# Performance work log

Measured on AMD Instinct MI355X. Metric: run time of the kernel, lower is better.

## Reference

```python
import jax, jax.numpy as jnp
import numpy as np

B, V = 4, 10242
N = B * V            # 40968 packed vertices
E_PER = 30720        # edges per mesh
HID = 128


def _bilinear_sample(fm, grid):
    """pytorch3d vert_align core: grid_sample(align_corners=True, bilinear).
    fm: [B,C,H,W], grid: [B,V,2] xy in [-1,1] -> [B,V,C]."""
    b_, c_, h_, w_ = fm.shape
    x = (grid[..., 0] + 1.0) * 0.5 * (w_ - 1)
    y = (grid[..., 1] + 1.0) * 0.5 * (h_ - 1)
    x0f, y0f = jnp.floor(x), jnp.floor(y)
    wx1, wy1 = x - x0f, y - y0f
    wx0, wy0 = 1.0 - wx1, 1.0 - wy1
    x0 = jnp.clip(x0f, 0, w_ - 1).astype(jnp.int32)
    x1 = jnp.clip(x0f + 1, 0, w_ - 1).astype(jnp.int32)
    y0 = jnp.clip(y0f, 0, h_ - 1).astype(jnp.int32)
    y1 = jnp.clip(y0f + 1, 0, h_ - 1).astype(jnp.int32)
    fmt = jnp.transpose(fm, (0, 2, 3, 1))  # [B,H,W,C]
    bi = jnp.arange(b_)[:, None]
    g = lambda yy, xx: fmt[bi, yy, xx]     # [B,V,C]
    return ((wy0 * wx0)[..., None] * g(y0, x0)
            + (wy0 * wx1)[..., None] * g(y0, x1)
            + (wy1 * wx0)[..., None] * g(y1, x0)
            + (wy1 * wx1)[..., None] * g(y1, x1))


def _graph_conv(x, edges, w0, b0, w1, b1):
    """pytorch3d GraphConv (undirected): W0 x_i + sum over both edge dirs of W1 x_j."""
    h0 = x @ w0 + b0
    h1 = x @ w1 + b1
    e0, e1 = edges[:, 0], edges[:, 1]
    agg = jnp.zeros_like(h0).at[e0].add(h1[e1]).at[e1].add(h1[e0])
    return h0 + agg


def setup_inputs() -> dict:
    key = jax.random.key(0)
    ks = jax.random.split(key, 20)
    s = 0.05
    # per-mesh edges, offset into packed index space
    e = jax.random.randint(ks[0], (B, E_PER, 2), 0, V)
    e = e + (jnp.arange(B) * V)[:, None, None]
    return {
        "feat1": jax.random.normal(ks[1], (B, 256, 56, 56), jnp.float32),
        "feat2": jax.random.normal(ks[2], (B, 512, 28, 28), jnp.float32),
        "feat3": jax.random.normal(ks[3], (B, 1024, 14, 14), jnp.float32),
        "feat4": jax.random.normal(ks[4], (B, 2048, 7, 7), jnp.float32),
        "aligned_verts": jax.random.uniform(ks[5], (B, V, 3), jnp.float32, -1.0, 1.0),
        "verts_packed": jax.random.normal(ks[6], (N, 3), jnp.float32),
        "image_enc": jax.random.normal(ks[7], (B, 256), jnp.float32),
        "edges": e.reshape(B * E_PER, 2).astype(jnp.int64),
        "bottleneck_w": jax.random.normal(ks[8], (3840, HID), jnp.float32) * s,
        "bottleneck_b": jnp.zeros((HID,), jnp.float32),
        "g0_w0": jax.random.normal(ks[9], (387, HID), jnp.float32) * s,
        "g0_b0": jnp.zeros((HID,), jnp.float32),
        "g0_w1": jax.random.normal(ks[10], (387, HID), jnp.float32) * s,
        "g0_b1": jnp.zeros((HID,), jnp.float32),
        "gw0": jax.random.normal(ks[11], (7, HID, HID), jnp.float32) * s,
        "gb0": jnp.zeros((7, HID), jnp.float32),
        "gw1": jax.random.normal(ks[12], (7, HID, HID), jnp.float32) * s,
        "gb1": jnp.zeros((7, HID), jnp.float32),
        "off_w": jax.random.normal(ks[13], (HID, 3), jnp.float32) * s,
        "off_b": jnp.zeros((3,), jnp.float32),
    }


def reference(feat1, feat2, feat3, feat4, aligned_verts, verts_packed, image_enc,
              edges, bottleneck_w, bottleneck_b, g0_w0, g0_b0, g0_w1, g0_b1,
              gw0, gb0, gw1, gb1, off_w, off_b):
    grid = aligned_verts[..., :2]  # vert_align uses xy only
    samp = jnp.concatenate([_bilinear_sample(f, grid)
                            for f in (feat1, feat2, feat3, feat4)], axis=-1)
    samp = samp.reshape(N, 3840)  # return_packed=True
    vfeat = jax.nn.relu(samp @ bottleneck_w + bottleneck_b)
    enc = jnp.repeat(image_enc, V, axis=0)  # repeat_interleave
    x = jnp.concatenate([vfeat, verts_packed, enc], axis=1)  # [N,387]
    x = jax.nn.relu(_graph_conv(x, edges, g0_w0, g0_b0, g0_w1, g0_b1))
    for i in range(7):
        x = jax.nn.relu(_graph_conv(x, edges, gw0[i], gb0[i], gw1[i], gb1[i]))
    return x @ off_w + off_b  # delta_v [N,3]
```

## Files before the change

### kernel.cpp

```cpp
#include <hip/hip_runtime.h>

static inline int ceil_div(int a, int b) { return (a + b - 1) / b; }

typedef __attribute__((ext_vector_type(8))) short short8;
typedef __attribute__((ext_vector_type(4))) float floatx4;

__device__ __forceinline__ unsigned short f2bf(float f) {
    unsigned int u = __float_as_uint(f);
    unsigned int r = (u + 0x7fffu + ((u >> 16) & 1u)) >> 16;
    return (unsigned short)r;
}
__device__ __forceinline__ float bf2f(unsigned short h) {
    return __uint_as_float(((unsigned int)h) << 16);
}

__global__ __launch_bounds__(1024) void scan1_k(const int* __restrict__ deg,
                                                int* __restrict__ excl,
                                                int* __restrict__ bsum, int Nv) {
    __shared__ int s[1024];
    int tid = threadIdx.x;
    int i = blockIdx.x * 1024 + tid;
    int v = (i < Nv) ? deg[i] : 0;
    s[tid] = v;
    __syncthreads();
    for (int off = 1; off < 1024; off <<= 1) {
        int t = (tid >= off) ? s[tid - off] : 0;
        __syncthreads();
        if (tid >= off) s[tid] += t;
        __syncthreads();
    }
    if (i < Nv) excl[i] = s[tid] - v;
    if (tid == 1023) bsum[blockIdx.x] = s[1023];
}

__global__ __launch_bounds__(1024) void scan3_k(const int* __restrict__ excl,
                                                const int* __restrict__ bsum,
                                                const int* __restrict__ deg,
                                                int* __restrict__ rowptr,
                                                int* __restrict__ cursor, int Nv, int nb) {
    __shared__ int offS;
    if (threadIdx.x < 64) {
        int v = (threadIdx.x < min((int)blockIdx.x, nb)) ? bsum[threadIdx.x] : 0;
#pragma unroll
        for (int m = 1; m < 64; m <<= 1) v += __shfl_xor(v, m);
        if (threadIdx.x == 0) offS = v;
    }
    __syncthreads();
    int i = blockIdx.x * 1024 + threadIdx.x;
    if (i < Nv) {
        int val = excl[i] + offS;
        rowptr[i] = val;
        cursor[i] = val;
        if (i == Nv - 1) rowptr[Nv] = val + deg[i];
    }
}

__global__ __launch_bounds__(256) void fill_adj_k(const int* __restrict__ edges,
                                                  int* __restrict__ cursor,
                                                  int* __restrict__ adj, int E) {
    int e = blockIdx.x * blockDim.x + threadIdx.x;
    if (e < E) {
        int a = edges[2 * e], b = edges[2 * e + 1];
        adj[atomicAdd(&cursor[a], 1)] = b;
        adj[atomicAdd(&cursor[b], 1)] = a;
    }
}

__global__ __launch_bounds__(256) void fatpre_k(
    const int* __restrict__ edges, int* __restrict__ deg, int E, int nE,
    const float* __restrict__ g0w0, const float* __restrict__ g0w1,
    const float* __restrict__ gw0, const float* __restrict__ gw1,
    unsigned short* __restrict__ Wt, const float* __restrict__ bw,
    unsigned short* __restrict__ bwT, const float* __restrict__ enc,
    float* __restrict__ encp, const float* __restrict__ fm1, const float* __restrict__ fm2,
    const float* __restrict__ fm3, const float* __restrict__ fm4,
    unsigned short* __restrict__ ft1, unsigned short* __restrict__ ft2,
    unsigned short* __restrict__ ft3, unsigned short* __restrict__ ft4, int B_) {
    __shared__ float tl[64][65];
    int bid = blockIdx.x;
    int tid = threadIdx.x;
    if (bid < nE) {
        int e = bid * 256 + tid;
        if (e < E) {
            atomicAdd(&deg[edges[2 * e]], 1);
            atomicAdd(&deg[edges[2 * e + 1]], 1);
        }
    } else if (bid < nE + 16) {
        int lh = bid - nE;
        int l = lh >> 1, h = lh & 1;
        const float* src;
        if (l == 0) src = h ? g0w1 : g0w0;
        else src = (h ? gw1 : gw0) + (size_t)(l - 1) * 16384;
        unsigned short* dst = Wt + (size_t)lh * 16384;
        for (int idx = tid; idx < 16384; idx += 256) {
            int n = idx >> 7, k = idx & 127;
            dst[n * 128 + k] = f2bf(src[k * 128 + n]);
        }
    } else if (bid < nE + 46) {
        int blk = bid - nE - 16;
        for (int idx = tid; idx < 16384; idx += 256) {
            int n = idx >> 7, kk = idx & 127;
            bwT[(size_t)n * 3840 + blk * 128 + kk] =
                f2bf(bw[(size_t)(blk * 128 + kk) * 128 + n]);
        }
    } else if (bid < nE + 46 + B_) {
        int b = bid - nE - 46;
        int sH = tid >> 7;
        int j = tid & 127;
        const float* w = sH ? g0w1 : g0w0;
        const float* eb = enc + b * 256;
        float acc = 0.f;
        for (int c = 0; c < 256; ++c) acc = fmaf(eb[c], w[(131 + c) * 128 + j], acc);
        encp[(sH * B_ + b) * 128 + j] = acc;
    } else {
        int idx = bid - (nE + 46 + B_);
        const float* fm;
        unsigned short* ft;
        int C, HW, PT, CT;
        int q1 = 49 * 4 * B_, q2 = 13 * 8 * B_, q3 = 4 * 16 * B_;
        if (idx < q1) {
            fm = fm1; ft = ft1; C = 256; HW = 3136; PT = 49; CT = 4;
        } else if ((idx -= q1) < q2) {
            fm = fm2; ft = ft2; C = 512; HW = 784; PT = 13; CT = 8;
        } else if ((idx -= q2) < q3) {
            fm = fm3; ft = ft3; C = 1024; HW = 196; PT = 4; CT = 16;
        } else {
            idx -= q3;
            fm = fm4; ft = ft4; C = 2048; HW = 49; PT = 1; CT = 32;
        }
        int ct = idx % CT;
        int r2 = idx / CT;
        int pt = r2 % PT;
        int b = r2 / PT;
        int p0 = pt * 64, c0 = ct * 64;
        const float* fb = fm + (size_t)b * C * HW;
#pragma unroll
        for (int l = 0; l < 4; ++l) {
            int i = tid + l * 256;
            int ch = i >> 4;
            int pq = (i & 15) * 4;
            const float* src = fb + (size_t)(c0 + ch) * HW + p0 + pq;
            float4 v;
            if (p0 + pq + 3 < HW) {
                v = *(const float4*)src;
            } else {
                v.x = (p0 + pq + 0 < HW) ? src[0] : 0.f;
                v.y = (p0 + pq + 1 < HW) ? src[1] : 0.f;
                v.z = (p0 + pq + 2 < HW) ? src[2] : 0.f;
                v.w = (p0 + pq + 3 < HW) ? src[3] : 0.f;
            }
            tl[ch][pq + 0] = v.x;
            tl[ch][pq + 1] = v.y;
            tl[ch][pq + 2] = v.z;
            tl[ch][pq + 3] = v.w;
        }
        __syncthreads();
#pragma unroll
        for (int l = 0; l < 2; ++l) {
            int i = tid + l * 256;
            int p = i >> 3;
            int cc = (i & 7) * 8;
            if (p0 + p < HW) {
                short8 o;
#pragma unroll
                for (int j = 0; j < 8; ++j) o[j] = (short)f2bf(tl[cc + j][p]);
                *(short8*)(ft + ((size_t)b * HW + p0 + p) * C + c0 + cc) = o;
            }
        }
    }
}

__global__ __launch_bounds__(256) void proj_all_k(
    const unsigned short* __restrict__ ft1, const unsigned short* __restrict__ ft2,
    const unsigned short* __restrict__ ft3, const unsigned short* __restrict__ ft4,
    const unsigned short* __restrict__ bwT, float* __restrict__ o1, float* __restrict__ o2,
    float* __restrict__ o3, float* __restrict__ o4, int B_) {
    __shared__ unsigned short wlds[8192];

    int tid = threadIdx.x;
    int n1 = 49 * B_ * 2, n2 = 13 * B_ * 2, n3 = 4 * B_ * 4;
    int bid = blockIdx.x;
    const unsigned short* ft;
    float* op;
    int C, HW, PT, idx, koff, KB;
    if (bid < n1) {
        ft = ft1; op = o1; C = 256; HW = 3136; PT = 49; idx = bid; koff = 0; KB = 128;
    } else if (bid < n1 + n2) {
        ft = ft2; op = o2; C = 512; HW = 784; PT = 13; idx = bid - n1; koff = 256; KB = 256;
    } else if (bid < n1 + n2 + n3) {
        ft = ft3; op = o3; C = 1024; HW = 196; PT = 4; idx = bid - n1 - n2; koff = 768;
        KB = 256;
    } else {
        ft = ft4; op = o4; C = 2048; HW = 49; PT = 1; idx = bid - n1 - n2 - n3; koff = 1792;
        KB = 256;
    }
    int pt = idx % PT;
    int r2 = idx / PT;
    int b = r2 % B_;
    int zz = r2 / B_;
    int p0 = pt * 64;
    int kcf0 = zz * KB;

    int wave = tid >> 6, lane = tid & 63;
    int row16 = lane & 15, quad = lane >> 4;
    int p = p0 + wave * 16 + row16;
    bool pok = (p < HW);
    int pc = pok ? p : (HW - 1);
    const unsigned short* frow = ft + ((size_t)b * HW + pc) * C;

    floatx4 acc[8];
#pragma unroll
    for (int j = 0; j < 8; ++j) acc[j] = (floatx4){0.f, 0.f, 0.f, 0.f};

    int nzz = KB >> 6;
    for (int zz2 = 0; zz2 < nzz; ++zz2) {
        int kcf = kcf0 + zz2 * 64;
        int kcw = koff + kcf;
        if (zz2) __syncthreads();
#pragma unroll
        for (int l = 0; l < 4; ++l) {
            int i2 = tid + l * 256;
            int n = i2 >> 3, c16 = i2 & 7;
            *(short8*)&wlds[n * 64 + ((c16 ^ (n & 7)) * 8)] =
                *(const short8*)(bwT + (size_t)n * 3840 + kcw + c16 * 8);
        }
        short8 ax[2];
#pragma unroll
        for (int ks = 0; ks < 2; ++ks)
            ax[ks] = *(const short8*)(frow + kcf + ks * 32 + quad * 8);
        __syncthreads();
#pragma unroll
        for (int ks = 0; ks < 2; ++ks) {
            int c = ks * 4 + quad;
#pragma unroll
            for (int nt = 0; nt < 8; ++nt) {
                int wr = nt * 16 + row16;
                short8 bwf = *(short8*)&wlds[wr * 64 + ((c ^ (wr & 7)) * 8)];
                acc[nt] =
                    __builtin_amdgcn_mfma_f32_16x16x32_bf16(ax[ks], bwf, acc[nt], 0, 0, 0);
            }
        }
    }

    float* obase = op + (size_t)b * HW * 128;
#pragma unroll
    for (int nt = 0; nt < 8; ++nt) {
        int colg = nt * 16 + row16;
#pragma unroll
        for (int rr = 0; rr < 4; ++rr) {
            int pr = p0 + wave * 16 + quad * 4 + rr;
            if (pr < HW) atomicAdd(&obase[(size_t)pr * 128 + colg], acc[nt][rr]);
        }
    }
}

__device__ __forceinline__ void sample2(const float* __restrict__ pp, int Hh, int Ww,
                                        float gx, float gy, int c2, float& a0, float& a1) {
    float x = (gx + 1.f) * 0.5f * (float)(Ww - 1);
    float y = (gy + 1.f) * 0.5f * (float)(Hh - 1);
    float x0f = floorf(x), y0f = floorf(y);
    float wx1 = x - x0f, wy1 = y - y0f;
    float wx0 = 1.f - wx1, wy0 = 1.f - wy1;
    int x0 = (int)fminf(fmaxf(x0f, 0.f), (float)(Ww - 1));
    int x1 = (int)fminf(fmaxf(x0f + 1.f, 0.f), (float)(Ww - 1));
    int y0 = (int)fminf(fmaxf(y0f, 0.f), (float)(Hh - 1));
    int y1 = (int)fminf(fmaxf(y0f + 1.f, 0.f), (float)(Hh - 1));
    float2 r00 = *(const float2*)(pp + (size_t)(y0 * Ww + x0) * 128 + c2);
    float2 r01 = *(const float2*)(pp + (size_t)(y0 * Ww + x1) * 128 + c2);
    float2 r10 = *(const float2*)(pp + (size_t)(y1 * Ww + x0) * 128 + c2);
    float2 r11 = *(const float2*)(pp + (size_t)(y1 * Ww + x1) * 128 + c2);
    a0 += wy0 * (wx0 * r00.x + wx1 * r01.x) + wy1 * (wx0 * r10.x + wx1 * r11.x);
    a1 += wy0 * (wx0 * r00.y + wx1 * r01.y) + wy1 * (wx0 * r10.y + wx1 * r11.y);
}

__global__ __launch_bounds__(256) void sample_bottleneck_k(
    const float* __restrict__ av, const float* __restrict__ pp1, const float* __restrict__ pp2,
    const float* __restrict__ pp3, const float* __restrict__ pp4, const float* __restrict__ bb,
    const float* __restrict__ verts, const float* __restrict__ encp,
    const float* __restrict__ g0w0, const float* __restrict__ g0w1,
    const float* __restrict__ g0b0, const float* __restrict__ g0b1,
    unsigned short* __restrict__ X, unsigned short* __restrict__ H, int Nv, int V_, int B_) {
    int wave = threadIdx.x >> 6, lane = threadIdx.x & 63;
    int n = blockIdx.x * 4 + wave;
    if (n >= Nv) return;
    int b = n / V_;
    int c2 = 2 * lane;
    float gx = av[(size_t)n * 3 + 0];
    float gy = av[(size_t)n * 3 + 1];
    float2 bbv = *(const float2*)(bb + c2);
    float a0 = bbv.x, a1 = bbv.y;
    sample2(pp1 + (size_t)b * 3136 * 128, 56, 56, gx, gy, c2, a0, a1);
    sample2(pp2 + (size_t)b * 784 * 128, 28, 28, gx, gy, c2, a0, a1);
    sample2(pp3 + (size_t)b * 196 * 128, 14, 14, gx, gy, c2, a0, a1);
    sample2(pp4 + (size_t)b * 49 * 128, 7, 7, gx, gy, c2, a0, a1);
    *(unsigned int*)(X + (size_t)n * 128 + c2) =
        (unsigned int)f2bf(fmaxf(a0, 0.f)) | ((unsigned int)f2bf(fmaxf(a1, 0.f)) << 16);

    float v0 = verts[n * 3 + 0], v1 = verts[n * 3 + 1], v2 = verts[n * 3 + 2];
    float2 e0 = *(const float2*)(encp + ((size_t)(0 * B_ + b)) * 128 + c2);
    float2 e1 = *(const float2*)(encp + ((size_t)(1 * B_ + b)) * 128 + c2);
    float2 gb0v = *(const float2*)(g0b0 + c2);
    float2 gb1v = *(const float2*)(g0b1 + c2);
    float2 w0a = *(const float2*)(g0w0 + 128 * 128 + c2);
    float2 w0b = *(const float2*)(g0w0 + 129 * 128 + c2);
    float2 w0c = *(const float2*)(g0w0 + 130 * 128 + c2);
    float2 w1a = *(const float2*)(g0w1 + 128 * 128 + c2);
    float2 w1b = *(const float2*)(g0w1 + 129 * 128 + c2);
    float2 w1c = *(const float2*)(g0w1 + 130 * 128 + c2);
    float h0x = e0.x + gb0v.x + v0 * w0a.x + v1 * w0b.x + v2 * w0c.x;
    float h0y = e0.y + gb0v.y + v0 * w0a.y + v1 * w0b.y + v2 * w0c.y;
    float h1x = e1.x + gb1v.x + v0 * w1a.x + v1 * w1b.x + v2 * w1c.x;
    float h1y = e1.y + gb1v.y + v0 * w1a.y + v1 * w1b.y + v2 * w1c.y;
    *(unsigned int*)(H + (size_t)n * 256 + c2) =
        (unsigned int)f2bf(h0x) | ((unsigned int)f2bf(h0y) << 16);
    *(unsigned int*)(H + (size_t)n * 256 + 128 + c2) =
        (unsigned int)f2bf(h1x) | ((unsigned int)f2bf(h1y) << 16);
}

__global__ __launch_bounds__(256) void agg0_k(const unsigned short* __restrict__ X,
                                              const unsigned short* __restrict__ H,
                                              const int* __restrict__ rowptr,
                                              const int* __restrict__ adj,
                                              unsigned short* __restrict__ AggX,
                                              unsigned short* __restrict__ AggH, int Nv,
                                              int Etot) {
    int wave = threadIdx.x >> 6, lane = threadIdx.x & 63;
    int n0 = (blockIdx.x * 4 + wave) * 4;
    if (n0 >= Nv) return;
    int g = lane >> 4, c = lane & 15;
    int rp = rowptr[min(n0 + (lane & 7), Nv)];
    int sg = __shfl(rp, g);
    int eg = __shfl(rp, g + 1);
    int m = eg - sg;
    m = max(m, __shfl_xor(m, 16));
    m = max(m, __shfl_xor(m, 32));

    int n = n0 + g;
    bool nok = (n < Nv);
    int nc = nok ? n : (Nv - 1);
    float accx[8], acch[8];
    short8 h0v = *(const short8*)(H + (size_t)nc * 256 + c * 8);
#pragma unroll
    for (int j = 0; j < 8; ++j) {
        accx[j] = 0.f;
        acch[j] = bf2f((unsigned short)h0v[j]);
    }

    for (int it = 0; it < m; it += 8) {
        int t = sg + it + (lane & 7);
        int adjv = adj[min(t, Etot - 1)];
        short8 bx[8], bh[8];
#pragma unroll
        for (int q = 0; q < 8; ++q) {
            int nbq = __shfl(adjv, (lane & 48) + q);
            bx[q] = *(const short8*)(X + (size_t)nbq * 128 + c * 8);
            bh[q] = *(const short8*)(H + (size_t)nbq * 256 + 128 + c * 8);
        }
#pragma unroll
        for (int q = 0; q < 8; ++q) {
            bool ok = (sg + it + q < eg);
#pragma unroll
            for (int j = 0; j < 8; ++j) {
                accx[j] += ok ? bf2f((unsigned short)bx[q][j]) : 0.f;
                acch[j] += ok ? bf2f((unsigned short)bh[q][j]) : 0.f;
            }
        }
    }
    if (nok) {
        short8 ox, oh;
#pragma unroll
        for (int j = 0; j < 8; ++j) {
            ox[j] = (short)f2bf(accx[j]);
            oh[j] = (short)f2bf(acch[j]);
        }
        *(short8*)(AggX + (size_t)n * 128 + c * 8) = ox;
        *(short8*)(AggH + (size_t)n * 128 + c * 8) = oh;
    }
}

__global__ __launch_bounds__(256) void agg_x_k(const unsigned short* __restrict__ X,
                                               const int* __restrict__ rowptr,
                                               const int* __restrict__ adj,
                                               unsigned short* __restrict__ Agg, int Nv,
                                               int Etot) {
    int wave = threadIdx.x >> 6, lane = threadIdx.x & 63;
    int n0 = (blockIdx.x * 4 + wave) * 4;
    if (n0 >= Nv) return;
    int g = lane >> 4, c = lane & 15;
    int rp = rowptr[min(n0 + (lane & 7), Nv)];
    int sg = __shfl(rp, g);
    int eg = __shfl(rp, g + 1);
    int m = eg - sg;
    m = max(m, __shfl_xor(m, 16));
    m = max(m, __shfl_xor(m, 32));

    float acc[8];
#pragma unroll
    for (int j = 0; j < 8; ++j) acc[j] = 0.f;

    for (int it = 0; it < m; it += 8) {
        int t = sg + it + (lane & 7);
        int adjv = adj[min(t, Etot - 1)];
        short8 buf[8];
#pragma unroll
        for (int q = 0; q < 8; ++q) {
            int nbq = __shfl(adjv, (lane & 48) + q);
            buf[q] = *(const short8*)(X + (size_t)nbq * 128 + c * 8);
        }
#pragma unroll
        for (int q = 0; q < 8; ++q) {
            bool ok = (sg + it + q < eg);
#pragma unroll
            for (int j = 0; j < 8; ++j) {
                float v = bf2f((unsigned short)buf[q][j]);
                acc[j] += ok ? v : 0.f;
            }
        }
    }

    if (n0 + g < Nv) {
        short8 o;
#pragma unroll
        for (int j = 0; j < 8; ++j) o[j] = (short)f2bf(acc[j]);
        *(short8*)(Agg + (size_t)(n0 + g) * 128 + c * 8) = o;
    }
}

__global__ __launch_bounds__(256, 3) void gemm_dual_k(
    const unsigned short* __restrict__ Xin, const unsigned short* __restrict__ Agg,
    const unsigned short* __restrict__ Wt,
    const float* __restrict__ b0, const float* __restrict__ b1,
    const unsigned short* __restrict__ aggh, const int* __restrict__ degv,
    unsigned short* __restrict__ Xout, int M, const float* __restrict__ ow,
    const float* __restrict__ ob, float* __restrict__ outp) {
    __shared__ unsigned short wlds[16384];
    __shared__ unsigned short cs[64 * 72];
    __shared__ float bS[128];
    __shared__ float owS[192];

    int tid = threadIdx.x;
    int m0 = blockIdx.x * 128;
    int yb = blockIdx.y;

    int wave = tid >> 6, lane = tid & 63;
    int row16 = lane & 15;
    int quad = lane >> 4;
    int wrow = wave * 16;

    short8 axT[2][4], agT[2][4];
    int dgT[2][4];
    {
        int g = min(m0 + wrow + row16, M - 1);
#pragma unroll
        for (int ks = 0; ks < 4; ++ks) {
            int koff = ks * 32 + quad * 8;
            axT[0][ks] = *(const short8*)(Xin + (size_t)g * 128 + koff);
            agT[0][ks] = *(const short8*)(Agg + (size_t)g * 128 + koff);
        }
#pragma unroll
        for (int rr = 0; rr < 4; ++rr)
            dgT[0][rr] = degv[min(m0 + wrow + quad * 4 + rr, M - 1)];
    }

    if (tid < 64) {
        bS[tid] = b0 ? b0[yb * 64 + tid] : 0.f;
        bS[64 + tid] = b1 ? b1[yb * 64 + tid] : 0.f;
    }
    if (outp && tid < 192) owS[tid] = ow[yb * 192 + tid];

    const unsigned short* W0h = Wt + (size_t)yb * 64 * 128;
    const unsigned short* W1h = Wt + 16384 + (size_t)yb * 64 * 128;
#pragma unroll
    for (int l = 0; l < 8; ++l) {
        int idx = tid + l * 256;
        int half = idx >> 10;
        int r = (idx >> 4) & 63;
        int c16 = idx & 15;
        int sw = (c16 ^ (r & 15)) * 8;
        const unsigned short* src = (half ? W1h : W0h) + r * 128 + c16 * 8;
        *(short8*)&wlds[half * 8192 + r * 128 + sw] = *(const short8*)src;
    }
    __syncthreads();

    {
        int g = min(m0 + 64 + wrow + row16, M - 1);
#pragma unroll
        for (int ks = 0; ks < 4; ++ks) {
            int koff = ks * 32 + quad * 8;
            axT[1][ks] = *(const short8*)(Xin + (size_t)g * 128 + koff);
            agT[1][ks] = *(const short8*)(Agg + (size_t)g * 128 + koff);
        }
#pragma unroll
        for (int rr = 0; rr < 4; ++rr)
            dgT[1][rr] = degv[min(m0 + 64 + wrow + quad * 4 + rr, M - 1)];
    }

#pragma unroll
    for (int t = 0; t < 2; ++t) {
        int mT = m0 + t * 64;
        floatx4 acc[4];
#pragma unroll
        for (int j = 0; j < 4; j++) acc[j] = (floatx4){0.f, 0.f, 0.f, 0.f};

#pragma unroll
        for (int ks = 0; ks < 4; ++ks) {
            int c = ks * 4 + quad;
#pragma unroll
            for (int nt = 0; nt < 4; ++nt) {
                int wr = nt * 16 + row16;
                short8 bw0 = *(short8*)&wlds[wr * 128 + ((c ^ row16) * 8)];
                short8 bw1 = *(short8*)&wlds[8192 + wr * 128 + ((c ^ row16) * 8)];
                acc[nt] = __builtin_amdgcn_mfma_f32_16x16x32_bf16(axT[t][ks], bw0, acc[nt], 0, 0, 0);
                acc[nt] = __builtin_amdgcn_mfma_f32_16x16x32_bf16(agT[t][ks], bw1, acc[nt], 0, 0, 0);
            }
        }

        unsigned short cvs[4][4];
#pragma unroll
        for (int nt = 0; nt < 4; ++nt) {
            int colh = nt * 16 + row16;
            int colg = yb * 64 + colh;
            float bc0 = bS[colh];
            float bc1 = bS[64 + colh];
#pragma unroll
            for (int rr = 0; rr < 4; ++rr) {
                int row = wrow + quad * 4 + rr;
                int gm = mT + row;
                float v = acc[nt][rr] + bc0 + (float)dgT[t][rr] * bc1;
                if (aggh && gm < M) v += bf2f(aggh[(size_t)gm * 128 + colg]);
                unsigned short cv = f2bf(fmaxf(v, 0.f));
                cvs[nt][rr] = cv;
                cs[row * 72 + colh] = cv;
            }
        }

        if (outp) {
#pragma unroll
            for (int rr = 0; rr < 4; ++rr) {
                float h0 = 0.f, h1 = 0.f, h2 = 0.f;
#pragma unroll
                for (int nt = 0; nt < 4; ++nt) {
                    int colh = nt * 16 + row16;
                    float xv = bf2f(cvs[nt][rr]);
                    h0 += xv * owS[colh * 3 + 0];
                    h1 += xv * owS[colh * 3 + 1];
                    h2 += xv * owS[colh * 3 + 2];
                }
#pragma unroll
                for (int mm = 1; mm < 16; mm <<= 1) {
                    h0 += __shfl_xor(h0, mm);
                    h1 += __shfl_xor(h1, mm);
                    h2 += __shfl_xor(h2, mm);
                }
                if (row16 == 0) {
                    int gm = mT + wrow + quad * 4 + rr;
                    if (gm < M) {
                        float e0 = (yb == 0) ? ob[0] : 0.f;
                        float e1 = (yb == 0) ? ob[1] : 0.f;
                        float e2 = (yb == 0) ? ob[2] : 0.f;
                        atomicAdd(&outp[gm * 3 + 0], h0 + e0);
                        atomicAdd(&outp[gm * 3 + 1], h1 + e1);
                        atomicAdd(&outp[gm * 3 + 2], h2 + e2);
                    }
                }
            }
        }
        __syncthreads();

        {
            int r = tid >> 2;
            int cq = (tid & 3) * 16;
            int gm = mT + r;
            if (gm < M) {
                unsigned short* dst = Xout + (size_t)gm * 128 + yb * 64 + cq;
                *(short8*)dst = *(short8*)&cs[r * 72 + cq];
                *(short8*)(dst + 8) = *(short8*)&cs[r * 72 + cq + 8];
            }
        }
        __syncthreads();
    }
}

extern "C" void kernel_launch(void* const* d_in, const int* in_sizes, int n_in, void* d_out,
                              int out_size, void* d_ws, size_t ws_size, hipStream_t stream) {
    const float* feat1 = (const float*)d_in[0];
    const float* feat2 = (const float*)d_in[1];
    const float* feat3 = (const float*)d_in[2];
    const float* feat4 = (const float*)d_in[3];
    const float* av = (const float*)d_in[4];
    const float* verts = (const float*)d_in[5];
    const float* image_enc = (const float*)d_in[6];
    const int* edges = (const int*)d_in[7];
    const float* bw = (const float*)d_in[8];
    const float* bb = (const float*)d_in[9];
    const float* g0w0 = (const float*)d_in[10];
    const float* g0b0 = (const float*)d_in[11];
    const float* g0w1 = (const float*)d_in[12];
    const float* g0b1 = (const float*)d_in[13];
    const float* gw0 = (const float*)d_in[14];
    const float* gb0 = (const float*)d_in[15];
    const float* gw1 = (const float*)d_in[16];
    const float* gb1 = (const float*)d_in[17];
    const float* off_w = (const float*)d_in[18];
    const float* off_b = (const float*)d_in[19];

    int B_ = in_sizes[6] / 256;
    int N_ = in_sizes[5] / 3;
    int V_ = N_ / B_;
    int E_ = in_sizes[7] / 2;

    char* wsb = (char*)d_ws;
    size_t off = 0;
    auto alloc = [&](size_t bytes) -> void* {
        void* p = (void*)(wsb + off);
        off += (bytes + 255) & ~(size_t)255;
        return p;
    };
    int S1 = B_ * 3136 * 128;
    int S2 = B_ * 784 * 128;
    int S3 = B_ * 196 * 128;
    int S4 = B_ * 49 * 128;
    float* pp1 = (float*)alloc((size_t)S1 * 4);
    float* pp2 = (float*)alloc((size_t)S2 * 4);
    float* pp3 = (float*)alloc((size_t)S3 * 4);
    float* pp4 = (float*)alloc((size_t)S4 * 4);
    size_t pp_bytes = off;
    unsigned short* fmT1 = (unsigned short*)alloc((size_t)B_ * 3136 * 256 * 2);
    unsigned short* fmT2 = (unsigned short*)alloc((size_t)B_ * 784 * 512 * 2);
    unsigned short* fmT3 = (unsigned short*)alloc((size_t)B_ * 196 * 1024 * 2);
    unsigned short* fmT4 = (unsigned short*)alloc((size_t)B_ * 49 * 2048 * 2);
    unsigned short* XA = (unsigned short*)alloc((size_t)N_ * 128 * 2);
    unsigned short* XB = (unsigned short*)alloc((size_t)N_ * 128 * 2);
    unsigned short* AggB = (unsigned short*)alloc((size_t)N_ * 128 * 2);
    unsigned short* AggH = (unsigned short*)alloc((size_t)N_ * 128 * 2);
    unsigned short* Hb = (unsigned short*)alloc((size_t)N_ * 256 * 2);
    unsigned short* Wt = (unsigned short*)alloc((size_t)8 * 2 * 128 * 128 * 2);
    unsigned short* bwT = (unsigned short*)alloc((size_t)128 * 3840 * 2);
    float* encp = (float*)alloc((size_t)2 * B_ * 128 * 4);
    int* deg = (int*)alloc((size_t)(N_ + 1) * 4);
    int* rowptr = (int*)alloc((size_t)(N_ + 1) * 4);
    int* cursor = (int*)alloc((size_t)N_ * 4);
    int* excl = (int*)alloc((size_t)N_ * 4);
    int* bsum = (int*)alloc((size_t)64 * 4);
    int* adj = (int*)alloc((size_t)2 * E_ * 4);

    hipMemsetAsync(deg, 0, (N_ + 1) * sizeof(int), stream);
    hipMemsetAsync(wsb, 0, pp_bytes, stream);
    hipMemsetAsync(d_out, 0, out_size, stream);

    int nE = ceil_div(E_, 256);
    int NT = (49 * 4 + 13 * 8 + 4 * 16 + 1 * 32) * B_;
    fatpre_k<<<nE + 46 + B_ + NT, 256, 0, stream>>>(
        edges, deg, E_, nE, g0w0, g0w1, gw0, gw1, Wt, bw, bwT, image_enc, encp, feat1, feat2,
        feat3, feat4, fmT1, fmT2, fmT3, fmT4, B_);

    int nb = ceil_div(N_, 1024);
    scan1_k<<<nb, 1024, 0, stream>>>(deg, excl, bsum, N_);
    scan3_k<<<nb, 1024, 0, stream>>>(excl, bsum, deg, rowptr, cursor, N_, nb);
    fill_adj_k<<<ceil_div(E_, 256), 256, 0, stream>>>(edges, cursor, adj, E_);

    int nproj = 49 * B_ * 2 + 13 * B_ * 2 + 4 * B_ * 4 + 1 * B_ * 8;
    proj_all_k<<<nproj, 256, 0, stream>>>(fmT1, fmT2, fmT3, fmT4, bwT, pp1, pp2, pp3, pp4,
                                          B_);

    sample_bottleneck_k<<<ceil_div(N_, 4), 256, 0, stream>>>(
        av, pp1, pp2, pp3, pp4, bb, verts, encp, g0w0, g0w1, g0b0, g0b1, XA, Hb, N_, V_, B_);

    dim3 ggrid(ceil_div(N_, 128), 2);
    int agrid4 = ceil_div(N_, 16);
    agg0_k<<<agrid4, 256, 0, stream>>>(XA, Hb, rowptr, adj, AggB, AggH, N_, 2 * E_);
    gemm_dual_k<<<ggrid, 256, 0, stream>>>(XA, AggB, Wt, nullptr, nullptr, AggH, deg, XB, N_,
                                           nullptr, nullptr, nullptr);
    unsigned short* Xc = XB;
    unsigned short* Xn = XA;
    for (int i = 0; i < 7; ++i) {
        bool last = (i == 6);
        agg_x_k<<<agrid4, 256, 0, stream>>>(Xc, rowptr, adj, AggB, N_, 2 * E_);
        gemm_dual_k<<<ggrid, 256, 0, stream>>>(Xc, AggB, Wt + (size_t)(i + 1) * 32768,
                                               gb0 + i * 128, gb1 + i * 128, nullptr, deg, Xn,
                                               N_, last ? off_w : nullptr,
                                               last ? off_b : nullptr,
                                               last ? (float*)d_out : nullptr);
        unsigned short* t = Xc;
        Xc = Xn;
        Xn = t;
    }
}
```

Measured before the change: 436.1 us.

## Fuse seven graph-conv layers into one cooperative persistent kernel with grid syncs

Replaces the 14 separate aggregation and GEMM launches for layers 1-7 with a single cooperative kernel. It loops over the layers and separates the aggregation and GEMM phases with grid-wide syncs, using grid-stride loops over chunks and tiles. This removes per-launch overhead and the inter-kernel gaps. The trade-off is a grid limited by occupancy, grid-sync cost, and weights reloaded into LDS for every tile a block handles.

Measured after the change: 990.9 us. 127% more time.

```diff
diff --git a/kernel.cpp b/kernel.cpp
--- a/kernel.cpp
+++ b/kernel.cpp
@@ -1,4 +1,7 @@
 #include <hip/hip_runtime.h>
+#include <hip/hip_cooperative_groups.h>
+
+namespace cg = cooperative_groups;
 
 static inline int ceil_div(int a, int b) { return (a + b - 1) / b; }
 
@@ -378,65 +381,15 @@
     }
 }
 
-__global__ __launch_bounds__(256) void agg_x_k(const unsigned short* __restrict__ X,
-                                               const int* __restrict__ rowptr,
-                                               const int* __restrict__ adj,
-                                               unsigned short* __restrict__ Agg, int Nv,
-                                               int Etot) {
-    int wave = threadIdx.x >> 6, lane = threadIdx.x & 63;
-    int n0 = (blockIdx.x * 4 + wave) * 4;
-    if (n0 >= Nv) return;
-    int g = lane >> 4, c = lane & 15;
-    int rp = rowptr[min(n0 + (lane & 7), Nv)];
-    int sg = __shfl(rp, g);
-    int eg = __shfl(rp, g + 1);
-    int m = eg - sg;
-    m = max(m, __shfl_xor(m, 16));
-    m = max(m, __shfl_xor(m, 32));
-
-    float acc[8];
-#pragma unroll
-    for (int j = 0; j < 8; ++j) acc[j] = 0.f;
-
-    for (int it = 0; it < m; it += 8) {
-        int t = sg + it + (lane & 7);
-        int adjv = adj[min(t, Etot - 1)];
-        short8 buf[8];
-#pragma unroll
-        for (int q = 0; q < 8; ++q) {
-            int nbq = __shfl(adjv, (lane & 48) + q);
-            buf[q] = *(const short8*)(X + (size_t)nbq * 128 + c * 8);
-        }
-#pragma unroll
-        for (int q = 0; q < 8; ++q) {
-            bool ok = (sg + it + q < eg);
-#pragma unroll
-            for (int j = 0; j < 8; ++j) {
-                float v = bf2f((unsigned short)buf[q][j]);
-                acc[j] += ok ? v : 0.f;
-            }
-        }
-    }
-
-    if (n0 + g < Nv) {
-        short8 o;
-#pragma unroll
-        for (int j = 0; j < 8; ++j) o[j] = (short)f2bf(acc[j]);
-        *(short8*)(Agg + (size_t)(n0 + g) * 128 + c * 8) = o;
-    }
-}
-
 __global__ __launch_bounds__(256, 3) void gemm_dual_k(
     const unsigned short* __restrict__ Xin, const unsigned short* __restrict__ Agg,
     const unsigned short* __restrict__ Wt,
     const float* __restrict__ b0, const float* __restrict__ b1,
     const unsigned short* __restrict__ aggh, const int* __restrict__ degv,
-    unsigned short* __restrict__ Xout, int M, const float* __restrict__ ow,
-    const float* __restrict__ ob, float* __restrict__ outp) {
+    unsigned short* __restrict__ Xout, int M) {
     __shared__ unsigned short wlds[16384];
     __shared__ unsigned short cs[64 * 72];
     __shared__ float bS[128];
-    __shared__ float owS[192];
 
     int tid = threadIdx.x;
     int m0 = blockIdx.x * 128;
@@ -466,7 +419,6 @@
         bS[tid] = b0 ? b0[yb * 64 + tid] : 0.f;
         bS[64 + tid] = b1 ? b1[yb * 64 + tid] : 0.f;
     }
-    if (outp && tid < 192) owS[tid] = ow[yb * 192 + tid];
 
     const unsigned short* W0h = Wt + (size_t)yb * 64 * 128;
     const unsigned short* W1h = Wt + 16384 + (size_t)yb * 64 * 128;
@@ -515,7 +467,6 @@
             }
         }
 
-        unsigned short cvs[4][4];
 #pragma unroll
         for (int nt = 0; nt < 4; ++nt) {
             int colh = nt * 16 + row16;
@@ -528,41 +479,7 @@
                 int gm = mT + row;
                 float v = acc[nt][rr] + bc0 + (float)dgT[t][rr] * bc1;
                 if (aggh && gm < M) v += bf2f(aggh[(size_t)gm * 128 + colg]);
-                unsigned short cv = f2bf(fmaxf(v, 0.f));
-                cvs[nt][rr] = cv;
-                cs[row * 72 + colh] = cv;
-            }
-        }
-
-        if (outp) {
-#pragma unroll
-            for (int rr = 0; rr < 4; ++rr) {
-                float h0 = 0.f, h1 = 0.f, h2 = 0.f;
-#pragma unroll
-                for (int nt = 0; nt < 4; ++nt) {
-                    int colh = nt * 16 + row16;
-                    float xv = bf2f(cvs[nt][rr]);
-                    h0 += xv * owS[colh * 3 + 0];
-                    h1 += xv * owS[colh * 3 + 1];
-                    h2 += xv * owS[colh * 3 + 2];
-                }
-#pragma unroll
-                for (int mm = 1; mm < 16; mm <<= 1) {
-                    h0 += __shfl_xor(h0, mm);
-                    h1 += __shfl_xor(h1, mm);
-                    h2 += __shfl_xor(h2, mm);
-                }
-                if (row16 == 0) {
-                    int gm = mT + wrow + quad * 4 + rr;
-                    if (gm < M) {
-                        float e0 = (yb == 0) ? ob[0] : 0.f;
-                        float e1 = (yb == 0) ? ob[1] : 0.f;
-                        float e2 = (yb == 0) ? ob[2] : 0.f;
-                        atomicAdd(&outp[gm * 3 + 0], h0 + e0);
-                        atomicAdd(&outp[gm * 3 + 1], h1 + e1);
-                        atomicAdd(&outp[gm * 3 + 2], h2 + e2);
-                    }
-                }
+                cs[row * 72 + colh] = f2bf(fmaxf(v, 0.f));
             }
         }
         __syncthreads();
@@ -578,6 +495,214 @@
             }
         }
         __syncthreads();
+    }
+}
+
+__global__ __launch_bounds__(256, 3) void layers_coop_k(
+    unsigned short* __restrict__ X0, unsigned short* __restrict__ X1,
+    const int* __restrict__ rowptr, const int* __restrict__ adj,
+    const unsigned short* __restrict__ Wtb, const float* __restrict__ gb0,
+    const float* __restrict__ gb1, unsigned short* __restrict__ Agg,
+    const int* __restrict__ degv, int M, int Etot, const float* __restrict__ ow,
+    const float* __restrict__ ob, float* __restrict__ outp) {
+    cg::grid_group gridg = cg::this_grid();
+    __shared__ unsigned short wlds[16384];
+    __shared__ unsigned short cs[64 * 72];
+    __shared__ float bS[128];
+    __shared__ float owS[192];
+
+    int tid = threadIdx.x;
+    int wave = tid >> 6, lane = tid & 63;
+    int row16 = lane & 15, quad = lane >> 4;
+    int wrow = wave * 16;
+    int nchunks = (M + 15) >> 4;
+    int ntiles = ((M + 127) >> 7) * 2;
+
+    for (int layer = 0; layer < 7; ++layer) {
+        const unsigned short* Xin = (layer & 1) ? X1 : X0;
+        unsigned short* Xout = (layer & 1) ? X0 : X1;
+        const unsigned short* Wt = Wtb + (size_t)(layer + 1) * 32768;
+        const float* b0 = gb0 + layer * 128;
+        const float* b1 = gb1 + layer * 128;
+        bool last = (layer == 6);
+
+        for (int chunk = blockIdx.x; chunk < nchunks; chunk += gridDim.x) {
+            int n0 = chunk * 16 + wave * 4;
+            if (n0 < M) {
+                int g = lane >> 4, c = lane & 15;
+                int rp = rowptr[min(n0 + (lane & 7), M)];
+                int sg = __shfl(rp, g);
+                int eg = __shfl(rp, g + 1);
+                int m = eg - sg;
+                m = max(m, __shfl_xor(m, 16));
+                m = max(m, __shfl_xor(m, 32));
+                float acc[8];
+#pragma unroll
+                for (int j = 0; j < 8; ++j) acc[j] = 0.f;
+                for (int it = 0; it < m; it += 8) {
+                    int t = sg + it + (lane & 7);
+                    int adjv = adj[min(t, Etot - 1)];
+                    short8 buf[8];
+#pragma unroll
+                    for (int q = 0; q < 8; ++q) {
+                        int nbq = __shfl(adjv, (lane & 48) + q);
+                        buf[q] = *(const short8*)(Xin + (size_t)nbq * 128 + c * 8);
+                    }
+#pragma unroll
+                    for (int q = 0; q < 8; ++q) {
+                        bool ok = (sg + it + q < eg);
+#pragma unroll
+                        for (int j = 0; j < 8; ++j)
+                            acc[j] += ok ? bf2f((unsigned short)buf[q][j]) : 0.f;
+                    }
+                }
+                if (n0 + g < M) {
+                    short8 o;
+#pragma unroll
+                    for (int j = 0; j < 8; ++j) o[j] = (short)f2bf(acc[j]);
+                    *(short8*)(Agg + (size_t)(n0 + g) * 128 + c * 8) = o;
+                }
+            }
+        }
+        gridg.sync();
+
+        for (int tile = blockIdx.x; tile < ntiles; tile += gridDim.x) {
+            int m0 = (tile >> 1) * 128;
+            int yb = tile & 1;
+
+            short8 axT[2][4], agT[2][4];
+            int dgT[2][4];
+            {
+                int g = min(m0 + wrow + row16, M - 1);
+#pragma unroll
+                for (int ks = 0; ks < 4; ++ks) {
+                    int koff = ks * 32 + quad * 8;
+                    axT[0][ks] = *(const short8*)(Xin + (size_t)g * 128 + koff);
+                    agT[0][ks] = *(const short8*)(Agg + (size_t)g * 128 + koff);
+                }
+#pragma unroll
+                for (int rr = 0; rr < 4; ++rr)
+                    dgT[0][rr] = degv[min(m0 + wrow + quad * 4 + rr, M - 1)];
+            }
+
+            if (tid < 64) {
+                bS[tid] = b0[yb * 64 + tid];
+                bS[64 + tid] = b1[yb * 64 + tid];
+            }
+            if (last && tid < 192) owS[tid] = ow[yb * 192 + tid];
+
+            const unsigned short* W0h = Wt + (size_t)yb * 64 * 128;
+            const unsigned short* W1h = Wt + 16384 + (size_t)yb * 64 * 128;
+#pragma unroll
+            for (int l = 0; l < 8; ++l) {
+                int idx = tid + l * 256;
+                int half = idx >> 10;
+                int r = (idx >> 4) & 63;
+                int c16 = idx & 15;
+                int sw = (c16 ^ (r & 15)) * 8;
+                const unsigned short* src = (half ? W1h : W0h) + r * 128 + c16 * 8;
+                *(short8*)&wlds[half * 8192 + r * 128 + sw] = *(const short8*)src;
+            }
+            __syncthreads();
+
+            {
+                int g = min(m0 + 64 + wrow + row16, M - 1);
+#pragma unroll
+                for (int ks = 0; ks < 4; ++ks) {
+                    int koff = ks * 32 + quad * 8;
+                    axT[1][ks] = *(const short8*)(Xin + (size_t)g * 128 + koff);
+                    agT[1][ks] = *(const short8*)(Agg + (size_t)g * 128 + koff);
+                }
+#pragma unroll
+                for (int rr = 0; rr < 4; ++rr)
+                    dgT[1][rr] = degv[min(m0 + 64 + wrow + quad * 4 + rr, M - 1)];
+            }
+
+#pragma unroll
+            for (int t = 0; t < 2; ++t) {
+                int mT = m0 + t * 64;
+                floatx4 acc[4];
+#pragma unroll
+                for (int j = 0; j < 4; j++) acc[j] = (floatx4){0.f, 0.f, 0.f, 0.f};
+
+#pragma unroll
+                for (int ks = 0; ks < 4; ++ks) {
+                    int c = ks * 4 + quad;
+#pragma unroll
+                    for (int nt = 0; nt < 4; ++nt) {
+                        int wr = nt * 16 + row16;
+                        short8 bw0 = *(short8*)&wlds[wr * 128 + ((c ^ row16) * 8)];
+                        short8 bw1 = *(short8*)&wlds[8192 + wr * 128 + ((c ^ row16) * 8)];
+                        acc[nt] = __builtin_amdgcn_mfma_f32_16x16x32_bf16(axT[t][ks], bw0,
+                                                                          acc[nt], 0, 0, 0);
+                        acc[nt] = __builtin_amdgcn_mfma_f32_16x16x32_bf16(agT[t][ks], bw1,
+                                                                          acc[nt], 0, 0, 0);
+                    }
+                }
+
+                unsigned short cvs[4][4];
+#pragma unroll
+                for (int nt = 0; nt < 4; ++nt) {
+                    int colh = nt * 16 + row16;
+                    float bc0 = bS[colh];
+                    float bc1 = bS[64 + colh];
+#pragma unroll
+                    for (int rr = 0; rr < 4; ++rr) {
+                        int row = wrow + quad * 4 + rr;
+                        float v = acc[nt][rr] + bc0 + (float)dgT[t][rr] * bc1;
+                        unsigned short cv = f2bf(fmaxf(v, 0.f));
+                        cvs[nt][rr] = cv;
+                        cs[row * 72 + colh] = cv;
+                    }
+                }
+
+                if (last) {
+#pragma unroll
+                    for (int rr = 0; rr < 4; ++rr) {
+                        float h0 = 0.f, h1 = 0.f, h2 = 0.f;
+#pragma unroll
+                        for (int nt = 0; nt < 4; ++nt) {
+                            int colh = nt * 16 + row16;
+                            float xv = bf2f(cvs[nt][rr]);
+                            h0 += xv * owS[colh * 3 + 0];
+                            h1 += xv * owS[colh * 3 + 1];
+                            h2 += xv * owS[colh * 3 + 2];
+                        }
+#pragma unroll
+                        for (int mm = 1; mm < 16; mm <<= 1) {
+                            h0 += __shfl_xor(h0, mm);
+                            h1 += __shfl_xor(h1, mm);
+                            h2 += __shfl_xor(h2, mm);
+                        }
+                        if (row16 == 0) {
+                            int gm = mT + wrow + quad * 4 + rr;
+                            if (gm < M) {
+                                float e0 = (yb == 0) ? ob[0] : 0.f;
+                                float e1 = (yb == 0) ? ob[1] : 0.f;
+                                float e2 = (yb == 0) ? ob[2] : 0.f;
+                                atomicAdd(&outp[gm * 3 + 0], h0 + e0);
+                                atomicAdd(&outp[gm * 3 + 1], h1 + e1);
+                                atomicAdd(&outp[gm * 3 + 2], h2 + e2);
+                            }
+                        }
+                    }
+                }
+                __syncthreads();
+
+                {
+                    int r = tid >> 2;
+                    int cq = (tid & 3) * 16;
+                    int gm = mT + r;
+                    if (gm < M) {
+                        unsigned short* dst = Xout + (size_t)gm * 128 + yb * 64 + cq;
+                        *(short8*)dst = *(short8*)&cs[r * 72 + cq];
+                        *(short8*)(dst + 8) = *(short8*)&cs[r * 72 + cq + 8];
+                    }
+                }
+                __syncthreads();
+            }
+        }
+        gridg.sync();
     }
 }
 
@@ -669,20 +794,27 @@
     dim3 ggrid(ceil_div(N_, 128), 2);
     int agrid4 = ceil_div(N_, 16);
     agg0_k<<<agrid4, 256, 0, stream>>>(XA, Hb, rowptr, adj, AggB, AggH, N_, 2 * E_);
-    gemm_dual_k<<<ggrid, 256, 0, stream>>>(XA, AggB, Wt, nullptr, nullptr, AggH, deg, XB, N_,
-                                           nullptr, nullptr, nullptr);
-    unsigned short* Xc = XB;
-    unsigned short* Xn = XA;
-    for (int i = 0; i < 7; ++i) {
-        bool last = (i == 6);
-        agg_x_k<<<agrid4, 256, 0, stream>>>(Xc, rowptr, adj, AggB, N_, 2 * E_);
-        gemm_dual_k<<<ggrid, 256, 0, stream>>>(Xc, AggB, Wt + (size_t)(i + 1) * 32768,
-                                               gb0 + i * 128, gb1 + i * 128, nullptr, deg, Xn,
-                                               N_, last ? off_w : nullptr,
-                                               last ? off_b : nullptr,
-                                               last ? (float*)d_out : nullptr);
-        unsigned short* t = Xc;
-        Xc = Xn;
-        Xn = t;
-    }
-}
+    gemm_dual_k<<<ggrid, 256, 0, stream>>>(XA, AggB, Wt, nullptr, nullptr, AggH, deg, XB, N_);
+
+    {
+        int maxb = 0;
+        hipOccupancyMaxActiveBlocksPerMultiprocessor(&maxb, layers_coop_k, 256, 0);
+        if (maxb < 1) maxb = 1;
+        int dev = 0;
+        hipGetDevice(&dev);
+        int ncu = 0;
+        hipDeviceGetAttribute(&ncu, hipDeviceAttributeMultiprocessorCount, dev);
+        if (ncu < 1) ncu = 256;
+        int G = maxb * ncu;
+        int nchunks = ceil_div(N_, 16);
+        if (G > nchunks) G = nchunks;
+
+        unsigned short* X0 = XB;
+        unsigned short* X1 = XA;
+        int Etot = 2 * E_;
+        float* outp = (float*)d_out;
+        void* cargs[] = {&X0,  &X1,   &rowptr, &adj,   &Wt, &gb0,    &gb1,
+                         &AggB, &deg, &N_,     &Etot,  &off_w, &off_b, &outp};
+        hipLaunchCooperativeKernel(layers_coop_k, dim3(G), dim3(256), cargs, 0, stream);
+    }
+}
```
